# Performance work log

Hardware: AMD Instinct MI355X
Metric: run time of the kernel (lower is better)

## Reference

```python
import jax, jax.numpy as jnp
import numpy as np

N = 50000      # nodes
E = 800000     # edges
XS = 64        # x_size
ES = 32        # edge_attr dim (in_size = XS + ES = 96)
OUT = 64       # out_size
H = 128        # hidden_size
EPS = 1e-5


def _lin_init(k, fan_in, fan_out):
    s = 1.0 / np.sqrt(fan_in)
    kw, kb = jax.random.split(k)
    w = jax.random.uniform(kw, (fan_in, fan_out), minval=-s, maxval=s, dtype=jnp.float32)
    b = jax.random.uniform(kb, (fan_out,), minval=-s, maxval=s, dtype=jnp.float32)
    return w, b


def setup_inputs() -> dict:
    key = jax.random.key(0)
    ks = jax.random.split(key, 12)
    x = jax.random.normal(ks[0], (N, XS), dtype=jnp.float32)
    edge_index = jax.random.randint(ks[1], (2, E), 0, N, dtype=jnp.int64)
    edge_attr = jax.random.normal(ks[2], (E, ES), dtype=jnp.float32)
    u = jax.random.normal(ks[3], (1, 8), dtype=jnp.float32)
    batch = jnp.zeros((N,), dtype=jnp.int64)
    # MLP1: (96->128) LReLU (128->128) LReLU (128->64) LReLU LN(64)
    m1w0, m1b0 = _lin_init(ks[4], XS + ES, H)
    m1w1, m1b1 = _lin_init(ks[5], H, H)
    m1w2, m1b2 = _lin_init(ks[6], H, OUT)
    ln1_g = jnp.ones((OUT,), jnp.float32); ln1_b = jnp.zeros((OUT,), jnp.float32)
    # MLP2: (128->128) LReLU (128->128) LReLU (128->64) LReLU LN(64)
    m2w0, m2b0 = _lin_init(ks[7], XS + OUT, H)
    m2w1, m2b1 = _lin_init(ks[8], H, H)
    m2w2, m2b2 = _lin_init(ks[9], H, OUT)
    ln2_g = jnp.ones((OUT,), jnp.float32); ln2_b = jnp.zeros((OUT,), jnp.float32)
    return dict(x=x, edge_index=edge_index, edge_attr=edge_attr, u=u, batch=batch,
                m1w0=m1w0, m1b0=m1b0, m1w1=m1w1, m1b1=m1b1, m1w2=m1w2, m1b2=m1b2,
                ln1_g=ln1_g, ln1_b=ln1_b,
                m2w0=m2w0, m2b0=m2b0, m2w1=m2w1, m2b1=m2b1, m2w2=m2w2, m2b2=m2b2,
                ln2_g=ln2_g, ln2_b=ln2_b)


def _lrelu(v):
    return jax.nn.leaky_relu(v, 0.01)


def _layernorm(v, g, b):
    mu = jnp.mean(v, axis=-1, keepdims=True)
    var = jnp.mean(jnp.square(v - mu), axis=-1, keepdims=True)
    return (v - mu) * jax.lax.rsqrt(var + EPS) * g + b


def _mlp(h, w0, b0, w1, b1, w2, b2, g, bn):
    h = _lrelu(h @ w0 + b0)
    h = _lrelu(h @ w1 + b1)
    h = _lrelu(h @ w2 + b2)          # activate_last=True
    return _layernorm(h, g, bn)      # layer_norm=True


def reference(x, edge_index, edge_attr, u, batch,
              m1w0, m1b0, m1w1, m1b1, m1w2, m1b2, ln1_g, ln1_b,
              m2w0, m2b0, m2w1, m2b1, m2w2, m2b2, ln2_g, ln2_b):
    row, col = edge_index[0], edge_index[1]
    # gather source nodes, concat edge features -> per-edge MLP
    h = jnp.concatenate([x[row], edge_attr], axis=1)            # [E, 96]
    h = _mlp(h, m1w0, m1b0, m1w1, m1b1, m1w2, m1b2, ln1_g, ln1_b)  # [E, 64]
    # scatter_mean over destination nodes
    agg = jax.ops.segment_sum(h, col, num_segments=N)           # [N, 64]
    cnt = jax.ops.segment_sum(jnp.ones((E,), h.dtype), col, num_segments=N)
    agg = agg / jnp.maximum(cnt, 1.0)[:, None]
    # node update MLP
    h2 = jnp.concatenate([x, agg], axis=1)                      # [N, 128]
    return _mlp(h2, m2w0, m2b0, m2w1, m2b1, m2w2, m2b2, ln2_g, ln2_b)
```

## Files before the change

### kernel.cpp

```cpp
#include <hip/hip_runtime.h>


#define NNODES 50000
#define NEDGES 800000
#define NTILES_E2 3125
#define NTILES_N2 196

typedef __bf16 bf16;
typedef __bf16 __attribute__((ext_vector_type(4))) bf16x4;
typedef __bf16 __attribute__((ext_vector_type(8))) bf16x8;
typedef float __attribute__((ext_vector_type(4))) f32x4;

__device__ __forceinline__ f32x4 mfma_bf16(bf16x8 a, bf16x8 b, f32x4 c) {
    return __builtin_amdgcn_mfma_f32_16x16x32_bf16(a, b, c, 0, 0, 0);
}

__global__ void prep_weights(const float* __restrict__ w10, const float* __restrict__ w11,
                             const float* __restrict__ w12, const float* __restrict__ w20,
                             const float* __restrict__ w21, const float* __restrict__ w22,
                             bf16* __restrict__ img) {
    int idx = blockIdx.x * 256 + threadIdx.x;
    float f;
    if (idx < 13312) {
        int n = idx / 104, k = idx % 104;
        f = (k < 96) ? w10[k * 128 + n] : 0.0f;
    } else if (idx < 30720) {
        int t = idx - 13312; int n = t / 136, k = t % 136;
        f = (k < 128) ? w11[k * 128 + n] : 0.0f;
    } else if (idx < 39424) {
        int t = idx - 30720; int n = t / 136, k = t % 136;
        f = (k < 128) ? w12[k * 64 + n] : 0.0f;
    } else if (idx < 56832) {
        int t = idx - 39424; int n = t / 136, k = t % 136;
        f = (k < 128) ? w20[k * 128 + n] : 0.0f;
    } else if (idx < 74240) {
        int t = idx - 56832; int n = t / 136, k = t % 136;
        f = (k < 128) ? w21[k * 128 + n] : 0.0f;
    } else if (idx < 82944) {
        int t = idx - 74240; int n = t / 136, k = t % 136;
        f = (k < 128) ? w22[k * 64 + n] : 0.0f;
    } else {
        return;
    }
    img[idx] = (bf16)f;
}

__global__ void hist_kernel(const int* __restrict__ col, int* __restrict__ hist) {
    int i = blockIdx.x * 512 + threadIdx.x;
    if (i < NEDGES) {
        int d = col[i];
        if ((unsigned)d < (unsigned)NNODES) atomicAdd(hist + d, 1);
    }
}

__global__ void scanA(const int* __restrict__ hist, int* __restrict__ off,
                      int* __restrict__ csum) {
    __shared__ int sd[512];
    int t = threadIdx.x, i = blockIdx.x * 512 + t;
    int v = (i < NNODES) ? hist[i] : 0;
    sd[t] = v;
    __syncthreads();
    for (int o2 = 1; o2 < 512; o2 <<= 1) {
        int x = (t >= o2) ? sd[t - o2] : 0;
        __syncthreads();
        sd[t] += x;
        __syncthreads();
    }
    if (i < NNODES) off[i] = sd[t] - v;
    if (t == 511) csum[blockIdx.x] = sd[511];
}

__global__ void scanB(int* __restrict__ csum) {
    __shared__ int sd[128];
    int t = threadIdx.x;
    int v = (t < 98) ? csum[t] : 0;
    sd[t] = v;
    __syncthreads();
    for (int o2 = 1; o2 < 128; o2 <<= 1) {
        int x = (t >= o2) ? sd[t - o2] : 0;
        __syncthreads();
        sd[t] += x;
        __syncthreads();
    }
    if (t < 98) csum[t] = sd[t] - v;
}

__global__ void scanC(int* __restrict__ off, const int* __restrict__ csum) {
    int i = blockIdx.x * 512 + threadIdx.x;
    if (i < NNODES) off[i] += csum[blockIdx.x];
}

__global__ void scatter_kernel(const int* __restrict__ eidx, int* __restrict__ off,
                               int* __restrict__ perm, int* __restrict__ rdS) {
    int i = blockIdx.x * 512 + threadIdx.x;
    if (i < NEDGES) {
        int r = eidx[i], d = eidx[NEDGES + i];
        if ((unsigned)d < (unsigned)NNODES && (unsigned)r < (unsigned)NNODES) {
            int pos = atomicAdd(off + d, 1);
            if ((unsigned)pos < (unsigned)NEDGES) {
                perm[pos] = i;
                rdS[pos] = (int)(((unsigned)r & 0xFFFFu) | ((unsigned)d << 16));
            }
        }
    }
}

__global__ __launch_bounds__(512, 2) void edge_mlp(
    const float* __restrict__ x, const int* __restrict__ perm,
    const int* __restrict__ rdS, const float* __restrict__ eattr,
    const bf16* __restrict__ wimg,
    const float* __restrict__ b0g, const float* __restrict__ b1g,
    const float* __restrict__ b2g, const float* __restrict__ lng,
    const float* __restrict__ lnb, float* __restrict__ agg) {
    __shared__ __align__(16) bf16 wall[39424];
    __shared__ __align__(16) bf16 buf[256 * 136];
    __shared__ float bs[448];
    __shared__ int dstile[256];

    const int tid = threadIdx.x;
    {
        const uint4* src = (const uint4*)wimg;
        uint4* dst = (uint4*)wall;
        for (int i = tid; i < 4928; i += 512) dst[i] = src[i];
    }
    if (tid < 128) { bs[tid] = b0g[tid]; bs[128 + tid] = b1g[tid]; }
    else if (tid < 192) {
        int t = tid - 128;
        bs[256 + t] = b2g[t]; bs[320 + t] = lng[t]; bs[384 + t] = lnb[t];
    }
    __syncthreads();

    const int lane = tid & 63;
    const int wv = tid >> 6;
    const int col16 = lane & 15;
    const int quad = lane >> 4;

    float b0r[8], b1r[8], b2r[4], gr[4], br[4];
#pragma unroll
    for (int i = 0; i < 8; i++) { b0r[i] = bs[i * 16 + col16]; b1r[i] = bs[128 + i * 16 + col16]; }
#pragma unroll
    for (int i = 0; i < 4; i++) {
        b2r[i] = bs[256 + i * 16 + col16];
        gr[i] = bs[320 + i * 16 + col16];
        br[i] = bs[384 + i * 16 + col16];
    }

    const bf16* w0t = wall;
    const bf16* w1t = wall + 13312;
    const bf16* w2t = wall + 30720;

    const f32x4 vzero = {0.0f, 0.0f, 0.0f, 0.0f};
    const int r0 = wv * 32 + col16;
    const int rw = wv * 32 + quad * 4;
    const int el = tid >> 1, half = tid & 1;
    const int G = gridDim.x;

    int tile = blockIdx.x;

    float4 xr[8], er[4];
    unsigned cv;
    {
        int s = tile * 256 + el;
        cv = (unsigned)rdS[s];
        int ce = perm[s];
        int r = (int)(cv & 0xFFFFu); if (r >= NNODES) r = 0;
        if ((unsigned)ce >= (unsigned)NEDGES) ce = 0;
        const float4* xs = (const float4*)(x + (size_t)r * 64) + half * 8;
        const float4* es = (const float4*)(eattr + (size_t)ce * 32) + half * 4;
#pragma unroll
        for (int j = 0; j < 8; j++) xr[j] = xs[j];
#pragma unroll
        for (int j = 0; j < 4; j++) er[j] = es[j];
    }
    unsigned nv; int ne;
    {
        int t1 = tile + G;
        int s = (t1 < NTILES_E2 ? t1 * 256 : 0) + el;
        nv = (unsigned)rdS[s];
        ne = perm[s];
    }

    for (; tile < NTILES_E2; tile += G) {
        {
            unsigned d = cv >> 16;
            if (half == 0) dstile[el] = (d < (unsigned)NNODES) ? (int)d : 0;
            bf16* arow = buf + el * 136;
#pragma unroll
            for (int j = 0; j < 8; j++) {
                float4 vv = xr[j];
                bf16x4 u = {(bf16)vv.x, (bf16)vv.y, (bf16)vv.z, (bf16)vv.w};
                *(bf16x4*)(arow + half * 32 + j * 4) = u;
            }
#pragma unroll
            for (int j = 0; j < 4; j++) {
                float4 vv = er[j];
                bf16x4 u = {(bf16)vv.x, (bf16)vv.y, (bf16)vv.z, (bf16)vv.w};
                *(bf16x4*)(arow + 64 + half * 16 + j * 4) = u;
            }
        }
        __syncthreads();

        {
            int t2 = tile + G;
            if (t2 < NTILES_E2) {
                int r = (int)(nv & 0xFFFFu); if (r >= NNODES) r = 0;
                int e = ne; if ((unsigned)e >= (unsigned)NEDGES) e = 0;
                const float4* xs = (const float4*)(x + (size_t)r * 64) + half * 8;
                const float4* es = (const float4*)(eattr + (size_t)e * 32) + half * 4;
#pragma unroll
                for (int j = 0; j < 8; j++) xr[j] = xs[j];
#pragma unroll
                for (int j = 0; j < 4; j++) er[j] = es[j];
            }
        }
        unsigned pv; int pe;
        {
            int t3 = tile + 2 * G;
            int s = (t3 < NTILES_E2 ? t3 * 256 : 0) + el;
            pv = (unsigned)rdS[s];
            pe = perm[s];
        }

        f32x4 acc1[2][8];
#pragma unroll
        for (int mt = 0; mt < 2; mt++)
#pragma unroll
            for (int nt = 0; nt < 8; nt++) acc1[mt][nt] = vzero;
#pragma unroll
        for (int ks = 0; ks < 3; ks++) {
            bf16x8 a0 = *(const bf16x8*)(buf + r0 * 136 + ks * 32 + quad * 8);
            bf16x8 a1 = *(const bf16x8*)(buf + (r0 + 16) * 136 + ks * 32 + quad * 8);
#pragma unroll
            for (int nt = 0; nt < 8; nt++) {
                bf16x8 b = *(const bf16x8*)(w0t + (nt * 16 + col16) * 104 + ks * 32 + quad * 8);
                acc1[0][nt] = mfma_bf16(a0, b, acc1[0][nt]);
                acc1[1][nt] = mfma_bf16(a1, b, acc1[1][nt]);
            }
        }
#pragma unroll
        for (int mt = 0; mt < 2; mt++)
#pragma unroll
            for (int nt = 0; nt < 8; nt++)
#pragma unroll
                for (int rg = 0; rg < 4; rg++) {
                    float v = acc1[mt][nt][rg] + b0r[nt];
                    v = (v > 0.0f) ? v : 0.01f * v;
                    buf[(rw + mt * 16 + rg) * 136 + nt * 16 + col16] = (bf16)v;
                }

        bf16x8 a2[2][4];
#pragma unroll
        for (int mt = 0; mt < 2; mt++)
#pragma unroll
            for (int ks = 0; ks < 4; ks++)
                a2[mt][ks] = *(const bf16x8*)(buf + (r0 + mt * 16) * 136 + ks * 32 + quad * 8);
        f32x4 acc2[2][8];
#pragma unroll
        for (int mt = 0; mt < 2; mt++)
#pragma unroll
            for (int nt = 0; nt < 8; nt++) acc2[mt][nt] = vzero;
#pragma unroll
        for (int ks = 0; ks < 4; ks++) {
#pragma unroll
            for (int nt = 0; nt < 8; nt++) {
                bf16x8 b = *(const bf16x8*)(w1t + (nt * 16 + col16) * 136 + ks * 32 + quad * 8);
                acc2[0][nt] = mfma_bf16(a2[0][ks], b, acc2[0][nt]);
                acc2[1][nt] = mfma_bf16(a2[1][ks], b, acc2[1][nt]);
            }
        }
#pragma unroll
        for (int mt = 0; mt < 2; mt++)
#pragma unroll
            for (int nt = 0; nt < 8; nt++)
#pragma unroll
                for (int rg = 0; rg < 4; rg++) {
                    float v = acc2[mt][nt][rg] + b1r[nt];
                    v = (v > 0.0f) ? v : 0.01f * v;
                    buf[(rw + mt * 16 + rg) * 136 + nt * 16 + col16] = (bf16)v;
                }

        bf16x8 a3[2][4];
#pragma unroll
        for (int mt = 0; mt < 2; mt++)
#pragma unroll
            for (int ks = 0; ks < 4; ks++)
                a3[mt][ks] = *(const bf16x8*)(buf + (r0 + mt * 16) * 136 + ks * 32 + quad * 8);
        f32x4 acc3[2][4];
#pragma unroll
        for (int mt = 0; mt < 2; mt++)
#pragma unroll
            for (int nt = 0; nt < 4; nt++) acc3[mt][nt] = vzero;
#pragma unroll
        for (int ks = 0; ks < 4; ks++) {
#pragma unroll
            for (int nt = 0; nt < 4; nt++) {
                bf16x8 b = *(const bf16x8*)(w2t + (nt * 16 + col16) * 136 + ks * 32 + quad * 8);
                acc3[0][nt] = mfma_bf16(a3[0][ks], b, acc3[0][nt]);
                acc3[1][nt] = mfma_bf16(a3[1][ks], b, acc3[1][nt]);
            }
        }

        int drA[2][4];
#pragma unroll
        for (int mt = 0; mt < 2; mt++)
#pragma unroll
            for (int rg = 0; rg < 4; rg++) {
                int c = dstile[rw + mt * 16 + rg];
                drA[mt][rg] = ((unsigned)c < (unsigned)NNODES) ? c : 0;
            }
        __syncthreads();

#pragma unroll
        for (int mt = 0; mt < 2; mt++) {
            float vals[4][4];
            float s1[4] = {0.f, 0.f, 0.f, 0.f}, s2[4] = {0.f, 0.f, 0.f, 0.f};
#pragma unroll
            for (int nt = 0; nt < 4; nt++)
#pragma unroll
                for (int rg = 0; rg < 4; rg++) {
                    float v = acc3[mt][nt][rg] + b2r[nt];
                    v = (v > 0.0f) ? v : 0.01f * v;
                    vals[nt][rg] = v;
                    s1[rg] += v;
                    s2[rg] += v * v;
                }
#pragma unroll
            for (int off2 = 1; off2 < 16; off2 <<= 1) {
#pragma unroll
                for (int rg = 0; rg < 4; rg++) {
                    s1[rg] += __shfl_xor(s1[rg], off2);
                    s2[rg] += __shfl_xor(s2[rg], off2);
                }
            }
            float o[4][4];
#pragma unroll
            for (int rg = 0; rg < 4; rg++) {
                float mu = s1[rg] * 0.015625f;
                float var = s2[rg] * 0.015625f - mu * mu;
                float rstd = rsqrtf(var + 1e-5f);
#pragma unroll
                for (int nt = 0; nt < 4; nt++)
                    o[nt][rg] = (vals[nt][rg] - mu) * rstd * gr[nt] + br[nt];
            }
            float run0 = o[0][0], run1 = o[1][0], run2 = o[2][0], run3 = o[3][0];
            int cur = drA[mt][0];
#pragma unroll
            for (int rg = 1; rg < 4; rg++) {
                if (drA[mt][rg] != cur) {
                    float* dst = agg + (size_t)cur * 64 + col16;
                    atomicAdd(dst, run0); atomicAdd(dst + 16, run1);
                    atomicAdd(dst + 32, run2); atomicAdd(dst + 48, run3);
                    run0 = o[0][rg]; run1 = o[1][rg]; run2 = o[2][rg]; run3 = o[3][rg];
                    cur = drA[mt][rg];
                } else {
                    run0 += o[0][rg]; run1 += o[1][rg]; run2 += o[2][rg]; run3 += o[3][rg];
                }
            }
            float* dst = agg + (size_t)cur * 64 + col16;
            atomicAdd(dst, run0); atomicAdd(dst + 16, run1);
            atomicAdd(dst + 32, run2); atomicAdd(dst + 48, run3);
        }

        cv = nv; nv = pv; ne = pe;
    }
}

__global__ __launch_bounds__(512, 2) void node_mlp(
    const float* __restrict__ x, const float* __restrict__ agg,
    const int* __restrict__ hist, const bf16* __restrict__ wimg,
    const float* __restrict__ b0g, const float* __restrict__ b1g,
    const float* __restrict__ b2g, const float* __restrict__ lng,
    const float* __restrict__ lnb, float* __restrict__ out) {
    __shared__ __align__(16) bf16 wall[43520];
    __shared__ __align__(16) bf16 buf[256 * 136];
    __shared__ float bs[448];

    const int tid = threadIdx.x;
    {
        const uint4* src = (const uint4*)wimg;
        uint4* dst = (uint4*)wall;
        for (int i = tid; i < 5440; i += 512) dst[i] = src[i];
    }
    if (tid < 128) { bs[tid] = b0g[tid]; bs[128 + tid] = b1g[tid]; }
    else if (tid < 192) {
        int t = tid - 128;
        bs[256 + t] = b2g[t]; bs[320 + t] = lng[t]; bs[384 + t] = lnb[t];
    }
    __syncthreads();

    const int lane = tid & 63;
    const int wv = tid >> 6;
    const int col16 = lane & 15;
    const int quad = lane >> 4;

    float b0r[8], b1r[8], b2r[4], gr[4], br[4];
#pragma unroll
    for (int i = 0; i < 8; i++) { b0r[i] = bs[i * 16 + col16]; b1r[i] = bs[128 + i * 16 + col16]; }
#pragma unroll
    for (int i = 0; i < 4; i++) {
        b2r[i] = bs[256 + i * 16 + col16];
        gr[i] = bs[320 + i * 16 + col16];
        br[i] = bs[384 + i * 16 + col16];
    }

    const bf16* w0t = wall;
    const bf16* w1t = wall + 17408;
    const bf16* w2t = wall + 34816;

    const f32x4 vzero = {0.0f, 0.0f, 0.0f, 0.0f};
    const int r0 = wv * 32 + col16;
    const int rw = wv * 32 + quad * 4;
    const int el = tid >> 1, half = tid & 1;
    const int G = gridDim.x;

    int tile = blockIdx.x;
    if (tile >= NTILES_N2) return;

    float4 xr[8], ar[8];
    int cc;
    {
        int i = tile * 256 + el;
        if (i >= NNODES) i = NNODES - 1;
        const float4* xs = (const float4*)(x + (size_t)i * 64) + half * 8;
        const float4* as = (const float4*)(agg + (size_t)i * 64) + half * 8;
#pragma unroll
        for (int j = 0; j < 8; j++) { xr[j] = xs[j]; ar[j] = as[j]; }
        cc = hist[i];
    }

    for (; tile < NTILES_N2; tile += G) {
        const int nbase = tile * 256;
        {
            float inv = 1.0f / (float)(cc > 1 ? cc : 1);
            bf16* arow = buf + el * 136;
#pragma unroll
            for (int j = 0; j < 8; j++) {
                float4 v = xr[j];
                bf16x4 u = {(bf16)v.x, (bf16)v.y, (bf16)v.z, (bf16)v.w};
                *(bf16x4*)(arow + half * 32 + j * 4) = u;
            }
#pragma unroll
            for (int j = 0; j < 8; j++) {
                float4 v = ar[j];
                bf16x4 u = {(bf16)(v.x * inv), (bf16)(v.y * inv), (bf16)(v.z * inv), (bf16)(v.w * inv)};
                *(bf16x4*)(arow + 64 + half * 32 + j * 4) = u;
            }
        }
        __syncthreads();

        {
            int t2 = tile + G;
            if (t2 < NTILES_N2) {
                int i = t2 * 256 + el;
                if (i >= NNODES) i = NNODES - 1;
                const float4* xs = (const float4*)(x + (size_t)i * 64) + half * 8;
                const float4* as = (const float4*)(agg + (size_t)i * 64) + half * 8;
#pragma unroll
                for (int j = 0; j < 8; j++) { xr[j] = xs[j]; ar[j] = as[j]; }
                cc = hist[i];
            }
        }

        f32x4 acc1[2][8];
#pragma unroll
        for (int mt = 0; mt < 2; mt++)
#pragma unroll
            for (int nt = 0; nt < 8; nt++) acc1[mt][nt] = vzero;
#pragma unroll
        for (int ks = 0; ks < 4; ks++) {
            bf16x8 a0 = *(const bf16x8*)(buf + r0 * 136 + ks * 32 + quad * 8);
            bf16x8 a1 = *(const bf16x8*)(buf + (r0 + 16) * 136 + ks * 32 + quad * 8);
#pragma unroll
            for (int nt = 0; nt < 8; nt++) {
                bf16x8 b = *(const bf16x8*)(w0t + (nt * 16 + col16) * 136 + ks * 32 + quad * 8);
                acc1[0][nt] = mfma_bf16(a0, b, acc1[0][nt]);
                acc1[1][nt] = mfma_bf16(a1, b, acc1[1][nt]);
            }
        }
#pragma unroll
        for (int mt = 0; mt < 2; mt++)
#pragma unroll
            for (int nt = 0; nt < 8; nt++)
#pragma unroll
                for (int rg = 0; rg < 4; rg++) {
                    float v = acc1[mt][nt][rg] + b0r[nt];
                    v = (v > 0.0f) ? v : 0.01f * v;
                    buf[(rw + mt * 16 + rg) * 136 + nt * 16 + col16] = (bf16)v;
                }

        bf16x8 a2[2][4];
#pragma unroll
        for (int mt = 0; mt < 2; mt++)
#pragma unroll
            for (int ks = 0; ks < 4; ks++)
                a2[mt][ks] = *(const bf16x8*)(buf + (r0 + mt * 16) * 136 + ks * 32 + quad * 8);
        f32x4 acc2[2][8];
#pragma unroll
        for (int mt = 0; mt < 2; mt++)
#pragma unroll
            for (int nt = 0; nt < 8; nt++) acc2[mt][nt] = vzero;
#pragma unroll
        for (int ks = 0; ks < 4; ks++) {
#pragma unroll
            for (int nt = 0; nt < 8; nt++) {
                bf16x8 b = *(const bf16x8*)(w1t + (nt * 16 + col16) * 136 + ks * 32 + quad * 8);
                acc2[0][nt] = mfma_bf16(a2[0][ks], b, acc2[0][nt]);
                acc2[1][nt] = mfma_bf16(a2[1][ks], b, acc2[1][nt]);
            }
        }
#pragma unroll
        for (int mt = 0; mt < 2; mt++)
#pragma unroll
            for (int nt = 0; nt < 8; nt++)
#pragma unroll
                for (int rg = 0; rg < 4; rg++) {
                    float v = acc2[mt][nt][rg] + b1r[nt];
                    v = (v > 0.0f) ? v : 0.01f * v;
                    buf[(rw + mt * 16 + rg) * 136 + nt * 16 + col16] = (bf16)v;
                }

        bf16x8 a3[2][4];
#pragma unroll
        for (int mt = 0; mt < 2; mt++)
#pragma unroll
            for (int ks = 0; ks < 4; ks++)
                a3[mt][ks] = *(const bf16x8*)(buf + (r0 + mt * 16) * 136 + ks * 32 + quad * 8);
        f32x4 acc3[2][4];
#pragma unroll
        for (int mt = 0; mt < 2; mt++)
#pragma unroll
            for (int nt = 0; nt < 4; nt++) acc3[mt][nt] = vzero;
#pragma unroll
        for (int ks = 0; ks < 4; ks++) {
#pragma unroll
            for (int nt = 0; nt < 4; nt++) {
                bf16x8 b = *(const bf16x8*)(w2t + (nt * 16 + col16) * 136 + ks * 32 + quad * 8);
                acc3[0][nt] = mfma_bf16(a3[0][ks], b, acc3[0][nt]);
                acc3[1][nt] = mfma_bf16(a3[1][ks], b, acc3[1][nt]);
            }
        }
        __syncthreads();

#pragma unroll
        for (int mt = 0; mt < 2; mt++) {
            float vals[4][4];
            float s1[4] = {0.f, 0.f, 0.f, 0.f}, s2[4] = {0.f, 0.f, 0.f, 0.f};
#pragma unroll
            for (int nt = 0; nt < 4; nt++)
#pragma unroll
                for (int rg = 0; rg < 4; rg++) {
                    float v = acc3[mt][nt][rg] + b2r[nt];
                    v = (v > 0.0f) ? v : 0.01f * v;
                    vals[nt][rg] = v;
                    s1[rg] += v;
                    s2[rg] += v * v;
                }
#pragma unroll
            for (int off2 = 1; off2 < 16; off2 <<= 1) {
#pragma unroll
                for (int rg = 0; rg < 4; rg++) {
                    s1[rg] += __shfl_xor(s1[rg], off2);
                    s2[rg] += __shfl_xor(s2[rg], off2);
                }
            }
#pragma unroll
            for (int rg = 0; rg < 4; rg++) {
                float mu = s1[rg] * 0.015625f;
                float var = s2[rg] * 0.015625f - mu * mu;
                float rstd = rsqrtf(var + 1e-5f);
                int i = nbase + rw + mt * 16 + rg;
                if (i < NNODES) {
#pragma unroll
                    for (int nt = 0; nt < 4; nt++) {
                        float o = (vals[nt][rg] - mu) * rstd * gr[nt] + br[nt];
                        out[(size_t)i * 64 + nt * 16 + col16] = o;
                    }
                }
            }
        }
    }
}

extern "C" void kernel_launch(void* const* d_in, const int* in_sizes, int n_in,
                              void* d_out, int out_size, void* d_ws, size_t ws_size,
                              hipStream_t stream) {
    (void)in_sizes; (void)n_in; (void)out_size; (void)ws_size;
    const float* x     = (const float*)d_in[0];
    const int*   eidx  = (const int*)d_in[1];
    const float* eattr = (const float*)d_in[2];
    const float* m1w0 = (const float*)d_in[5];
    const float* m1b0 = (const float*)d_in[6];
    const float* m1w1 = (const float*)d_in[7];
    const float* m1b1 = (const float*)d_in[8];
    const float* m1w2 = (const float*)d_in[9];
    const float* m1b2 = (const float*)d_in[10];
    const float* ln1g = (const float*)d_in[11];
    const float* ln1b = (const float*)d_in[12];
    const float* m2w0 = (const float*)d_in[13];
    const float* m2b0 = (const float*)d_in[14];
    const float* m2w1 = (const float*)d_in[15];
    const float* m2b1 = (const float*)d_in[16];
    const float* m2w2 = (const float*)d_in[17];
    const float* m2b2 = (const float*)d_in[18];
    const float* ln2g = (const float*)d_in[19];
    const float* ln2b = (const float*)d_in[20];

    char* ws = (char*)d_ws;
    float* agg  = (float*)ws;
    int*   hist = (int*)(ws + 12800000);
    int*   off  = (int*)(ws + 13000000);
    int*   csum = (int*)(ws + 13200000);
    int*   perm = (int*)(ws + 13200512);
    int*   rdS  = (int*)(ws + 16400512);
    bf16*  wimg = (bf16*)(ws + 19600512);

    hipMemsetAsync(d_ws, 0, 13000000, stream);
    prep_weights<<<324, 256, 0, stream>>>(m1w0, m1w1, m1w2, m2w0, m2w1, m2w2, wimg);
    hist_kernel<<<1563, 512, 0, stream>>>(eidx + NEDGES, hist);
    scanA<<<98, 512, 0, stream>>>(hist, off, csum);
    scanB<<<1, 128, 0, stream>>>(csum);
    scanC<<<98, 512, 0, stream>>>(off, csum);
    scatter_kernel<<<1563, 512, 0, stream>>>(eidx, off, perm, rdS);
    edge_mlp<<<256, 512, 0, stream>>>(x, perm, rdS, eattr, wimg, m1b0, m1b1, m1b2,
                                      ln1g, ln1b, agg);
    node_mlp<<<196, 512, 0, stream>>>(x, agg, hist, wimg + 39424,
                                      m2b0, m2b1, m2b2, ln2g, ln2b, (float*)d_out);
}
```

Baseline: 489.6 us.

## Shrink edge MLP blocks and read W0/W2 from global to cut LDS

Measured after the change: 512.1 us. 1.05x slower.

```diff
diff --git a/kernel.cpp b/kernel.cpp
--- a/kernel.cpp
+++ b/kernel.cpp
@@ -3,8 +3,8 @@
 
 #define NNODES 50000
 #define NEDGES 800000
-#define NTILES_E2 3125
-#define NTILES_N2 196
+#define NTILES_E 6250
+#define NTILES_N 196
 
 typedef __bf16 bf16;
 typedef __bf16 __attribute__((ext_vector_type(4))) bf16x4;
@@ -105,23 +105,23 @@
     }
 }
 
-__global__ __launch_bounds__(512, 2) void edge_mlp(
+__global__ __launch_bounds__(256) void edge_mlp(
     const float* __restrict__ x, const int* __restrict__ perm,
     const int* __restrict__ rdS, const float* __restrict__ eattr,
     const bf16* __restrict__ wimg,
     const float* __restrict__ b0g, const float* __restrict__ b1g,
     const float* __restrict__ b2g, const float* __restrict__ lng,
     const float* __restrict__ lnb, float* __restrict__ agg) {
-    __shared__ __align__(16) bf16 wall[39424];
-    __shared__ __align__(16) bf16 buf[256 * 136];
+    __shared__ __align__(16) bf16 w1l[17408];
+    __shared__ __align__(16) bf16 buf[128 * 136];
     __shared__ float bs[448];
-    __shared__ int dstile[256];
+    __shared__ int dstile[128];
 
     const int tid = threadIdx.x;
     {
-        const uint4* src = (const uint4*)wimg;
-        uint4* dst = (uint4*)wall;
-        for (int i = tid; i < 4928; i += 512) dst[i] = src[i];
+        const uint4* src = (const uint4*)(wimg + 13312);
+        uint4* dst = (uint4*)w1l;
+        for (int i = tid; i < 2176; i += 256) dst[i] = src[i];
     }
     if (tid < 128) { bs[tid] = b0g[tid]; bs[128 + tid] = b1g[tid]; }
     else if (tid < 192) {
@@ -145,9 +145,8 @@
         br[i] = bs[384 + i * 16 + col16];
     }
 
-    const bf16* w0t = wall;
-    const bf16* w1t = wall + 13312;
-    const bf16* w2t = wall + 30720;
+    const bf16* w0t = wimg;
+    const bf16* w2t = wimg + 30720;
 
     const f32x4 vzero = {0.0f, 0.0f, 0.0f, 0.0f};
     const int r0 = wv * 32 + col16;
@@ -160,7 +159,7 @@
     float4 xr[8], er[4];
     unsigned cv;
     {
-        int s = tile * 256 + el;
+        int s = tile * 128 + el;
         cv = (unsigned)rdS[s];
         int ce = perm[s];
         int r = (int)(cv & 0xFFFFu); if (r >= NNODES) r = 0;
@@ -175,12 +174,12 @@
     unsigned nv; int ne;
     {
         int t1 = tile + G;
-        int s = (t1 < NTILES_E2 ? t1 * 256 : 0) + el;
+        int s = (t1 < NTILES_E ? t1 * 128 : 0) + el;
         nv = (unsigned)rdS[s];
         ne = perm[s];
     }
 
-    for (; tile < NTILES_E2; tile += G) {
+    for (; tile < NTILES_E; tile += G) {
         {
             unsigned d = cv >> 16;
             if (half == 0) dstile[el] = (d < (unsigned)NNODES) ? (int)d : 0;
@@ -202,7 +201,7 @@
 
         {
             int t2 = tile + G;
-            if (t2 < NTILES_E2) {
+            if (t2 < NTILES_E) {
                 int r = (int)(nv & 0xFFFFu); if (r >= NNODES) r = 0;
                 int e = ne; if ((unsigned)e >= (unsigned)NEDGES) e = 0;
                 const float4* xs = (const float4*)(x + (size_t)r * 64) + half * 8;
@@ -216,7 +215,7 @@
         unsigned pv; int pe;
         {
             int t3 = tile + 2 * G;
-            int s = (t3 < NTILES_E2 ? t3 * 256 : 0) + el;
+            int s = (t3 < NTILES_E ? t3 * 128 : 0) + el;
             pv = (unsigned)rdS[s];
             pe = perm[s];
         }
@@ -263,7 +262,7 @@
         for (int ks = 0; ks < 4; ks++) {
 #pragma unroll
             for (int nt = 0; nt < 8; nt++) {
-                bf16x8 b = *(const bf16x8*)(w1t + (nt * 16 + col16) * 136 + ks * 32 + quad * 8);
+                bf16x8 b = *(const bf16x8*)(w1l + (nt * 16 + col16) * 136 + ks * 32 + quad * 8);
                 acc2[0][nt] = mfma_bf16(a2[0][ks], b, acc2[0][nt]);
                 acc2[1][nt] = mfma_bf16(a2[1][ks], b, acc2[1][nt]);
             }
@@ -414,7 +413,7 @@
     const int G = gridDim.x;
 
     int tile = blockIdx.x;
-    if (tile >= NTILES_N2) return;
+    if (tile >= NTILES_N) return;
 
     float4 xr[8], ar[8];
     int cc;
@@ -428,7 +427,7 @@
         cc = hist[i];
     }
 
-    for (; tile < NTILES_N2; tile += G) {
+    for (; tile < NTILES_N; tile += G) {
         const int nbase = tile * 256;
         {
             float inv = 1.0f / (float)(cc > 1 ? cc : 1);
@@ -450,7 +449,7 @@
 
         {
             int t2 = tile + G;
-            if (t2 < NTILES_N2) {
+            if (t2 < NTILES_N) {
                 int i = t2 * 256 + el;
                 if (i >= NNODES) i = NNODES - 1;
                 const float4* xs = (const float4*)(x + (size_t)i * 64) + half * 8;
@@ -621,8 +620,8 @@
     scanB<<<1, 128, 0, stream>>>(csum);
     scanC<<<98, 512, 0, stream>>>(off, csum);
     scatter_kernel<<<1563, 512, 0, stream>>>(eidx, off, perm, rdS);
-    edge_mlp<<<256, 512, 0, stream>>>(x, perm, rdS, eattr, wimg, m1b0, m1b1, m1b2,
-                                      ln1g, ln1b, agg);
+    edge_mlp<<<512, 256, 0, stream>>>(x, perm, rdS, eattr, wimg,
+                                      m1b0, m1b1, m1b2, ln1g, ln1b, agg);
     node_mlp<<<196, 512, 0, stream>>>(x, agg, hist, wimg + 39424,
                                       m2b0, m2b1, m2b2, ln2g, ln2b, (float*)d_out);
 }
```
